# Performance work log

Measured on AMD Instinct MI355X. Metric: run time of the kernel, lower is better.

The kernel has to match this reference:

```python
import jax, jax.numpy as jnp
import numpy as np


def setup_inputs() -> dict:
    key = jax.random.key(0)
    k1, k2, k3, k4, k5 = jax.random.split(key, 5)
    b, n, L, D, m = 8, 8192, 512, 128, 16
    x = jax.random.normal(k1, (b, n, L), dtype=jnp.float32)
    # attention MLP: Linear(L->D, no bias), Tanh, Linear(D->1, no bias)
    W1 = jax.random.normal(k2, (L, D), dtype=jnp.float32) / np.sqrt(L).astype(np.float32)
    W2 = jax.random.normal(k3, (D, 1), dtype=jnp.float32) / np.sqrt(D).astype(np.float32)
    batched_image_ids = jax.random.randint(k4, (b, n), 0, m)  # which image each packed token belongs to
    key_pad_mask = jax.random.bernoulli(k5, 0.1, (b, n))      # True = padding token
    return {"x": x, "W1": W1, "W2": W2,
            "batched_image_ids": batched_image_ids,
            "key_pad_mask": key_pad_mask,
            "max_queries": 16}


def reference(x, W1, W2, batched_image_ids, key_pad_mask, max_queries):
    # Attention scores per token: tanh(x W1) W2 -> [b, n, 1]
    A = jnp.tanh(x @ W1) @ W2
    A = jnp.swapaxes(A, -1, -2)  # [b, 1, n]
    b, n, d = x.shape
    # Per-image pooling mask: token j contributes to query i iff its image id == i and not padded
    image_id_arange = jnp.arange(max_queries)                                    # [m]
    attn_pool_mask = (image_id_arange[None, :, None] == batched_image_ids[:, None, :])
    attn_pool_mask = attn_pool_mask & (~key_pad_mask)[:, None, :]                # [b, m, n]
    neg = -jnp.finfo(A.dtype).max
    A = jnp.where(attn_pool_mask, jnp.broadcast_to(A, (b, max_queries, n)), neg)
    A = jax.nn.softmax(A, axis=-1)                                               # [b, m, n]
    out = jnp.einsum('bmn,bnd->bmd', A, x)                                       # pooled per image
    # num_images == max_queries for every bag -> is_images selects everything
    out = out.reshape(b * max_queries, d)
    return out
```

## Files before the change

kernel.cpp:

```cpp
#include <hip/hip_runtime.h>
#include <hip/hip_bf16.h>
#include <cstdint>
#include <cstddef>

typedef __attribute__((ext_vector_type(8))) short bf16x8;
typedef __attribute__((ext_vector_type(4))) float f32x4;

#define BATCH 8
#define NTOK 8192
#define LDIM 512
#define DDIM 128
#define NQ 16
#define NSEG 8
#define SEGLEN (NTOK / NSEG)

static __device__ __forceinline__ short f2bf(float f) {
  uint32_t u = __float_as_uint(f);
  uint32_t r = u + 0x7fffu + ((u >> 16) & 1u);
  return (short)(r >> 16);
}

static __device__ __forceinline__ bf16x8 cvt8(float4 a, float4 b) {
  bf16x8 o;
  o[0] = f2bf(a.x); o[1] = f2bf(a.y); o[2] = f2bf(a.z); o[3] = f2bf(a.w);
  o[4] = f2bf(b.x); o[5] = f2bf(b.y); o[6] = f2bf(b.z); o[7] = f2bf(b.w);
  return o;
}

static __device__ __forceinline__ unsigned int flipf(float v) {
  unsigned int u = __float_as_uint(v);
  return (u & 0x80000000u) ? ~u : (u | 0x80000000u);
}
static __device__ __forceinline__ float unflipf(unsigned int u) {
  return __uint_as_float((u & 0x80000000u) ? (u & 0x7fffffffu) : ~u);
}

static __device__ __forceinline__ bool is_pad(const void* pad, int byteFlag, int j) {
  return byteFlag ? (((const unsigned char*)pad)[j] != 0)
                  : (((const int*)pad)[j] != 0);
}

__global__ __launch_bounds__(256) void k_detect(const unsigned int* __restrict__ pad_raw,
                                                int* __restrict__ flag,
                                                unsigned int* __restrict__ gmax) {
  if (threadIdx.x < 128) gmax[threadIdx.x] = 0u;
  int any_gt1 = 0;
  for (int i = threadIdx.x; i < 16384; i += 256)
    if (pad_raw[i] > 1u) any_gt1 = 1;
  unsigned long long m = __ballot(any_gt1);
  __shared__ int s[4];
  if ((threadIdx.x & 63) == 0) s[threadIdx.x >> 6] = (m != 0ull) ? 1 : 0;
  __syncthreads();
  if (threadIdx.x == 0) flag[0] = (s[0] | s[1] | s[2] | s[3]);
}

__global__ void k0_wfrag(const float* __restrict__ W1, short* __restrict__ wfrag) {
  int tid = blockIdx.x * blockDim.x + threadIdx.x;
  if (tid >= 16 * 8 * 64) return;
  int l = tid & 63;
  int t = (tid >> 6) & 7;
  int c = tid >> 9;
  int kbase = c * 32 + (l >> 4) * 8;
  int col = t * 16 + (l & 15);
  bf16x8 frag;
#pragma unroll
  for (int i = 0; i < 8; ++i) frag[i] = f2bf(W1[(size_t)(kbase + i) * DDIM + col]);
  ((bf16x8*)wfrag)[tid] = frag;
}

__global__ __launch_bounds__(512, 4) void k1_scores(const float* __restrict__ x,
                                                    const short* __restrict__ wfrag,
                                                    const float* __restrict__ W2,
                                                    const int* __restrict__ ids,
                                                    const void* __restrict__ pad,
                                                    const int* __restrict__ flag,
                                                    float* __restrict__ A,
                                                    unsigned int* __restrict__ gmax) {
  __shared__ short ldsw[32768];
  __shared__ unsigned int qmax[16];
  const int tid = threadIdx.x, wave = tid >> 6, lane = tid & 63;
  const int rowBase = blockIdx.x * 128 + wave * 16;
  const int b = rowBase >> 13;
  const float* xp = x + (size_t)(rowBase + (lane & 15)) * LDIM + ((lane >> 4) * 8);
  if (tid < 16) qmax[tid] = 0u;

#define STAGE(h)                                                                              \
  {                                                                                           \
    const unsigned int* src_ = (const unsigned int*)wfrag + (h) * 16384;                      \
    _Pragma("unroll")                                                                         \
    for (int i = 0; i < 8; ++i) {                                                             \
      __builtin_amdgcn_global_load_lds(                                                       \
          (const __attribute__((address_space(1))) unsigned int*)(src_ + (i * 512 + tid) * 4),\
          (__attribute__((address_space(3))) unsigned int*)&ldsw[(i * 512 + wave * 64) * 8],  \
          16, 0, 0);                                                                          \
    }                                                                                         \
  }

#define ALOAD(dst, c)                                  \
  {                                                    \
    dst[0] = *(const float4*)(xp + (c) * 32);          \
    dst[1] = *(const float4*)(xp + (c) * 32 + 4);      \
  }

  f32x4 acc[8];
#pragma unroll
  for (int t = 0; t < 8; ++t) acc[t] = (f32x4){0.f, 0.f, 0.f, 0.f};
  float4 avbuf[2][2];

  STAGE(0);
  ALOAD(avbuf[0], 0);
  ALOAD(avbuf[1], 1);
  __syncthreads();

#pragma unroll
  for (int cc = 0; cc < 8; ++cc) {
    bf16x8 af = cvt8(avbuf[cc & 1][0], avbuf[cc & 1][1]);
    if (cc < 6) ALOAD(avbuf[cc & 1], cc + 2);
#pragma unroll
    for (int t = 0; t < 8; ++t) {
      bf16x8 bfr = *(const bf16x8*)&ldsw[((cc * 8 + t) * 64 + lane) * 8];
      acc[t] = __builtin_amdgcn_mfma_f32_16x16x32_bf16(af, bfr, acc[t], 0, 0, 0);
    }
  }
  ALOAD(avbuf[0], 8);
  ALOAD(avbuf[1], 9);
  __syncthreads();
  STAGE(1);
  __syncthreads();

#pragma unroll
  for (int cc = 0; cc < 8; ++cc) {
    bf16x8 af = cvt8(avbuf[cc & 1][0], avbuf[cc & 1][1]);
    if (cc < 6) ALOAD(avbuf[cc & 1], 10 + cc);
#pragma unroll
    for (int t = 0; t < 8; ++t) {
      bf16x8 bfr = *(const bf16x8*)&ldsw[((cc * 8 + t) * 64 + lane) * 8];
      acc[t] = __builtin_amdgcn_mfma_f32_16x16x32_bf16(af, bfr, acc[t], 0, 0, 0);
    }
  }
#undef STAGE
#undef ALOAD

  float w2v[8];
#pragma unroll
  for (int t = 0; t < 8; ++t) w2v[t] = W2[t * 16 + (lane & 15)];
  const int bfl = flag[0];
  float asum[4] = {0.f, 0.f, 0.f, 0.f};
#pragma unroll
  for (int t = 0; t < 8; ++t) {
#pragma unroll
    for (int r = 0; r < 4; ++r) {
      float h = 1.f - 2.f / (__expf(2.f * acc[t][r]) + 1.f);
      asum[r] += h * w2v[t];
    }
  }
#pragma unroll
  for (int m = 1; m < 16; m <<= 1) {
#pragma unroll
    for (int r = 0; r < 4; ++r) asum[r] += __shfl_xor(asum[r], m, 64);
  }
  if ((lane & 15) == 0) {
    int rb = rowBase + (lane >> 4) * 4;
#pragma unroll
    for (int r = 0; r < 4; ++r) {
      int row = rb + r;
      float v = asum[r];
      A[row] = v;
      if (!is_pad(pad, bfl, row)) atomicMax(&qmax[ids[row]], flipf(v));
    }
  }
  __syncthreads();
  if (tid < 16 && qmax[tid] != 0u) atomicMax(&gmax[(b << 4) + tid], qmax[tid]);
}

__global__ __launch_bounds__(256) void k3_pool(const float* __restrict__ x,
                                               const float* __restrict__ A,
                                               const int* __restrict__ ids,
                                               const void* __restrict__ pad,
                                               const int* __restrict__ flag,
                                               const unsigned int* __restrict__ gmax,
                                               float* __restrict__ partial,
                                               float* __restrict__ wsum) {
  int blk = blockIdx.x;
  int s = blk & 7, q = (blk >> 3) & 15, b = blk >> 7;
  int wave = threadIdx.x >> 6, lane = threadIdx.x & 63;
  int bfl = flag[0];
  __shared__ float w_lds[1024];
  __shared__ unsigned short j_lds[1024];
  __shared__ int cnt[4];
  __shared__ float wred[4];

  unsigned int mraw = gmax[(b << 4) + q];
  float mx = (mraw == 0u) ? 0.f : unflipf(mraw);
  const int base = b * NTOK;

  int wbase = wave * 256;
  int wpos = wbase;
  float wacc = 0.f;
#pragma unroll
  for (int g = 0; g < 4; ++g) {
    int j = s * SEGLEN + wave * 256 + g * 64 + lane;
    bool mem = (ids[base + j] == q) && !is_pad(pad, bfl, base + j);
    float wt = mem ? __expf(A[base + j] - mx) : 0.f;
    wacc += wt;
    unsigned long long mask = __ballot(mem);
    if (mem) {
      int pos = wpos + __popcll(mask & ((1ull << lane) - 1ull));
      w_lds[pos] = wt;
      j_lds[pos] = (unsigned short)j;
    }
    wpos += __popcll(mask);
  }
#pragma unroll
  for (int m = 1; m < 64; m <<= 1) wacc += __shfl_xor(wacc, m, 64);
  if (lane == 0) { cnt[wave] = wpos - wbase; wred[wave] = wacc; }
  __syncthreads();

  int c0 = threadIdx.x * 2;
  float ax = 0.f, ay = 0.f;
  for (int w = 0; w < 4; ++w) {
    int nw = cnt[w];
#pragma unroll 2
    for (int e = 0; e < nw; ++e) {
      float wt = w_lds[w * 256 + e];
      int j = j_lds[w * 256 + e];
      const float* xr = x + (size_t)(base + j) * LDIM + c0;
      ax += wt * xr[0];
      ay += wt * xr[1];
    }
  }
  size_t po = (size_t)blk * LDIM + c0;
  partial[po] = ax;
  partial[po + 1] = ay;
  if (threadIdx.x == 0) wsum[blk] = wred[0] + wred[1] + wred[2] + wred[3];
}

__global__ void k4_reduce(const float* __restrict__ partial, const float* __restrict__ wsum,
                          float* __restrict__ out) {
  int e = blockIdx.x * blockDim.x + threadIdx.x;
  if (e >= BATCH * NQ * LDIM) return;
  int bi = e >> 9, c = e & 511;
  float ps = 0.f, ws = 0.f;
#pragma unroll
  for (int t = 0; t < 8; ++t) {
    ps += partial[(size_t)(bi * 8 + t) * LDIM + c];
    ws += wsum[bi * 8 + t];
  }
  out[e] = (ws > 0.f) ? (ps / ws) : 0.f;
}

extern "C" void kernel_launch(void* const* d_in, const int* in_sizes, int n_in,
                              void* d_out, int out_size, void* d_ws, size_t ws_size,
                              hipStream_t stream) {
  const float* x = (const float*)d_in[0];
  const float* W1 = (const float*)d_in[1];
  const float* W2 = (const float*)d_in[2];
  const int* ids = (const int*)d_in[3];
  const void* pad = d_in[4];
  float* out = (float*)d_out;

  char* ws = (char*)d_ws;
  short* wfrag = (short*)ws;
  float* A = (float*)(ws + 131072);
  unsigned int* gmax = (unsigned int*)(ws + 393216);
  float* wsum = (float*)(ws + 393728);
  int* flag = (int*)(ws + 397824);
  float* partial = (float*)(ws + 397952);

  hipLaunchKernelGGL(k_detect, dim3(1), dim3(256), 0, stream, (const unsigned int*)pad, flag, gmax);
  hipLaunchKernelGGL(k0_wfrag, dim3(32), dim3(256), 0, stream, W1, wfrag);
  hipLaunchKernelGGL(k1_scores, dim3((BATCH * NTOK) / 128), dim3(512), 0, stream,
                     x, wfrag, W2, ids, pad, flag, A, gmax);
  hipLaunchKernelGGL(k3_pool, dim3(BATCH * NQ * NSEG), dim3(256), 0, stream,
                     x, A, ids, pad, flag, gmax, partial, wsum);
  hipLaunchKernelGGL(k4_reduce, dim3((BATCH * NQ * LDIM) / 256), dim3(256), 0, stream,
                     partial, wsum, out);
}
```

Before: 71.63 us.

## Merge setup kernels, quarter W1 staging for occupancy, vectorize pooling gather

Merges the pad-detect kernel into the W1 fragment kernel, removing one launch. The scores kernel now stages W1 in four 32KB quarters instead of two 64KB halves, halving its LDS footprint and raising launch bounds to 6 blocks/CU, at the cost of extra barriers. The pooling kernel compacts member tokens into one contiguous list and splits it across two thread groups that load x with float4 instead of two scalar loads. The reduce kernel then sums twice as many partial rows.

After: 70.67 us. Within noise of the previous version (-1.3%).

```diff
diff --git a/kernel.cpp b/kernel.cpp
--- a/kernel.cpp
+++ b/kernel.cpp
@@ -40,35 +40,37 @@
                   : (((const int*)pad)[j] != 0);
 }
 
-__global__ __launch_bounds__(256) void k_detect(const unsigned int* __restrict__ pad_raw,
+__global__ __launch_bounds__(256) void k0_wfrag(const float* __restrict__ W1,
+                                                short* __restrict__ wfrag,
+                                                const unsigned int* __restrict__ pad_raw,
                                                 int* __restrict__ flag,
                                                 unsigned int* __restrict__ gmax) {
-  if (threadIdx.x < 128) gmax[threadIdx.x] = 0u;
-  int any_gt1 = 0;
-  for (int i = threadIdx.x; i < 16384; i += 256)
-    if (pad_raw[i] > 1u) any_gt1 = 1;
-  unsigned long long m = __ballot(any_gt1);
-  __shared__ int s[4];
-  if ((threadIdx.x & 63) == 0) s[threadIdx.x >> 6] = (m != 0ull) ? 1 : 0;
-  __syncthreads();
-  if (threadIdx.x == 0) flag[0] = (s[0] | s[1] | s[2] | s[3]);
-}
-
-__global__ void k0_wfrag(const float* __restrict__ W1, short* __restrict__ wfrag) {
   int tid = blockIdx.x * blockDim.x + threadIdx.x;
-  if (tid >= 16 * 8 * 64) return;
-  int l = tid & 63;
-  int t = (tid >> 6) & 7;
-  int c = tid >> 9;
-  int kbase = c * 32 + (l >> 4) * 8;
-  int col = t * 16 + (l & 15);
-  bf16x8 frag;
-#pragma unroll
-  for (int i = 0; i < 8; ++i) frag[i] = f2bf(W1[(size_t)(kbase + i) * DDIM + col]);
-  ((bf16x8*)wfrag)[tid] = frag;
-}
-
-__global__ __launch_bounds__(512, 4) void k1_scores(const float* __restrict__ x,
+  if (tid < 16 * 8 * 64) {
+    int l = tid & 63;
+    int t = (tid >> 6) & 7;
+    int c = tid >> 9;
+    int kbase = c * 32 + (l >> 4) * 8;
+    int col = t * 16 + (l & 15);
+    bf16x8 frag;
+#pragma unroll
+    for (int i = 0; i < 8; ++i) frag[i] = f2bf(W1[(size_t)(kbase + i) * DDIM + col]);
+    ((bf16x8*)wfrag)[tid] = frag;
+  }
+  if (blockIdx.x == 0) {
+    if (threadIdx.x < 128) gmax[threadIdx.x] = 0u;
+    int any_gt1 = 0;
+    for (int i = threadIdx.x; i < 16384; i += 256)
+      if (pad_raw[i] > 1u) any_gt1 = 1;
+    unsigned long long m = __ballot(any_gt1);
+    __shared__ int s[4];
+    if ((threadIdx.x & 63) == 0) s[threadIdx.x >> 6] = (m != 0ull) ? 1 : 0;
+    __syncthreads();
+    if (threadIdx.x == 0) flag[0] = (s[0] | s[1] | s[2] | s[3]);
+  }
+}
+
+__global__ __launch_bounds__(512, 6) void k1_scores(const float* __restrict__ x,
                                                     const short* __restrict__ wfrag,
                                                     const float* __restrict__ W2,
                                                     const int* __restrict__ ids,
@@ -76,7 +78,7 @@
                                                     const int* __restrict__ flag,
                                                     float* __restrict__ A,
                                                     unsigned int* __restrict__ gmax) {
-  __shared__ short ldsw[32768];
+  __shared__ short ldsw[16384];
   __shared__ unsigned int qmax[16];
   const int tid = threadIdx.x, wave = tid >> 6, lane = tid & 63;
   const int rowBase = blockIdx.x * 128 + wave * 16;
@@ -84,11 +86,11 @@
   const float* xp = x + (size_t)(rowBase + (lane & 15)) * LDIM + ((lane >> 4) * 8);
   if (tid < 16) qmax[tid] = 0u;
 
-#define STAGE(h)                                                                              \
+#define STAGE(qd)                                                                             \
   {                                                                                           \
-    const unsigned int* src_ = (const unsigned int*)wfrag + (h) * 16384;                      \
+    const unsigned int* src_ = (const unsigned int*)wfrag + (qd) * 8192;                      \
     _Pragma("unroll")                                                                         \
-    for (int i = 0; i < 8; ++i) {                                                             \
+    for (int i = 0; i < 4; ++i) {                                                             \
       __builtin_amdgcn_global_load_lds(                                                       \
           (const __attribute__((address_space(1))) unsigned int*)(src_ + (i * 512 + tid) * 4),\
           (__attribute__((address_space(3))) unsigned int*)&ldsw[(i * 512 + wave * 64) * 8],  \
@@ -113,29 +115,22 @@
   __syncthreads();
 
 #pragma unroll
-  for (int cc = 0; cc < 8; ++cc) {
-    bf16x8 af = cvt8(avbuf[cc & 1][0], avbuf[cc & 1][1]);
-    if (cc < 6) ALOAD(avbuf[cc & 1], cc + 2);
-#pragma unroll
-    for (int t = 0; t < 8; ++t) {
-      bf16x8 bfr = *(const bf16x8*)&ldsw[((cc * 8 + t) * 64 + lane) * 8];
-      acc[t] = __builtin_amdgcn_mfma_f32_16x16x32_bf16(af, bfr, acc[t], 0, 0, 0);
-    }
-  }
-  ALOAD(avbuf[0], 8);
-  ALOAD(avbuf[1], 9);
-  __syncthreads();
-  STAGE(1);
-  __syncthreads();
-
-#pragma unroll
-  for (int cc = 0; cc < 8; ++cc) {
-    bf16x8 af = cvt8(avbuf[cc & 1][0], avbuf[cc & 1][1]);
-    if (cc < 6) ALOAD(avbuf[cc & 1], 10 + cc);
-#pragma unroll
-    for (int t = 0; t < 8; ++t) {
-      bf16x8 bfr = *(const bf16x8*)&ldsw[((cc * 8 + t) * 64 + lane) * 8];
-      acc[t] = __builtin_amdgcn_mfma_f32_16x16x32_bf16(af, bfr, acc[t], 0, 0, 0);
+  for (int qd = 0; qd < 4; ++qd) {
+#pragma unroll
+    for (int cc = 0; cc < 4; ++cc) {
+      const int c = qd * 4 + cc;
+      bf16x8 af = cvt8(avbuf[c & 1][0], avbuf[c & 1][1]);
+      if (c < 14) ALOAD(avbuf[c & 1], c + 2);
+#pragma unroll
+      for (int t = 0; t < 8; ++t) {
+        bf16x8 bfr = *(const bf16x8*)&ldsw[((cc * 8 + t) * 64 + lane) * 8];
+        acc[t] = __builtin_amdgcn_mfma_f32_16x16x32_bf16(af, bfr, acc[t], 0, 0, 0);
+      }
+    }
+    if (qd < 3) {
+      __syncthreads();
+      STAGE(qd + 1);
+      __syncthreads();
     }
   }
 #undef STAGE
@@ -185,53 +180,64 @@
   int s = blk & 7, q = (blk >> 3) & 15, b = blk >> 7;
   int wave = threadIdx.x >> 6, lane = threadIdx.x & 63;
   int bfl = flag[0];
-  __shared__ float w_lds[1024];
-  __shared__ unsigned short j_lds[1024];
+  __shared__ float w_u[1024];
+  __shared__ unsigned short j_u[1024];
   __shared__ int cnt[4];
   __shared__ float wred[4];
 
   unsigned int mraw = gmax[(b << 4) + q];
   float mx = (mraw == 0u) ? 0.f : unflipf(mraw);
   const int base = b * NTOK;
-
-  int wbase = wave * 256;
-  int wpos = wbase;
+  const int tokBase = s * SEGLEN + wave * 256;
+
+  int myCnt = 0;
+#pragma unroll
+  for (int g = 0; g < 4; ++g) {
+    int j = tokBase + g * 64 + lane;
+    bool mem = (ids[base + j] == q) && !is_pad(pad, bfl, base + j);
+    myCnt += __popcll(__ballot(mem));
+  }
+  if (lane == 0) cnt[wave] = myCnt;
+  __syncthreads();
+
+  int wpos = 0;
+#pragma unroll
+  for (int w = 0; w < 4; ++w) if (w < wave) wpos += cnt[w];
+  const int total = cnt[0] + cnt[1] + cnt[2] + cnt[3];
+
   float wacc = 0.f;
 #pragma unroll
   for (int g = 0; g < 4; ++g) {
-    int j = s * SEGLEN + wave * 256 + g * 64 + lane;
+    int j = tokBase + g * 64 + lane;
     bool mem = (ids[base + j] == q) && !is_pad(pad, bfl, base + j);
     float wt = mem ? __expf(A[base + j] - mx) : 0.f;
     wacc += wt;
     unsigned long long mask = __ballot(mem);
     if (mem) {
       int pos = wpos + __popcll(mask & ((1ull << lane) - 1ull));
-      w_lds[pos] = wt;
-      j_lds[pos] = (unsigned short)j;
+      w_u[pos] = wt;
+      j_u[pos] = (unsigned short)j;
     }
     wpos += __popcll(mask);
   }
 #pragma unroll
   for (int m = 1; m < 64; m <<= 1) wacc += __shfl_xor(wacc, m, 64);
-  if (lane == 0) { cnt[wave] = wpos - wbase; wred[wave] = wacc; }
-  __syncthreads();
-
-  int c0 = threadIdx.x * 2;
-  float ax = 0.f, ay = 0.f;
-  for (int w = 0; w < 4; ++w) {
-    int nw = cnt[w];
-#pragma unroll 2
-    for (int e = 0; e < nw; ++e) {
-      float wt = w_lds[w * 256 + e];
-      int j = j_lds[w * 256 + e];
-      const float* xr = x + (size_t)(base + j) * LDIM + c0;
-      ax += wt * xr[0];
-      ay += wt * xr[1];
-    }
-  }
-  size_t po = (size_t)blk * LDIM + c0;
-  partial[po] = ax;
-  partial[po + 1] = ay;
+  if (lane == 0) wred[wave] = wacc;
+  __syncthreads();
+
+  int grp = threadIdx.x >> 7, ct = threadIdx.x & 127;
+  int c0 = ct * 4;
+  int half = (total + 1) >> 1;
+  int e0 = grp ? half : 0;
+  int e1 = grp ? total : half;
+  float4 av = {0.f, 0.f, 0.f, 0.f};
+  for (int e = e0; e < e1; ++e) {
+    float wt = w_u[e];
+    int j = j_u[e];
+    float4 xr = *(const float4*)(x + (size_t)(base + j) * LDIM + c0);
+    av.x += wt * xr.x; av.y += wt * xr.y; av.z += wt * xr.z; av.w += wt * xr.w;
+  }
+  *(float4*)(partial + ((size_t)(blk * 2 + grp)) * LDIM + c0) = av;
   if (threadIdx.x == 0) wsum[blk] = wred[0] + wred[1] + wred[2] + wred[3];
 }
 
@@ -242,10 +248,9 @@
   int bi = e >> 9, c = e & 511;
   float ps = 0.f, ws = 0.f;
 #pragma unroll
-  for (int t = 0; t < 8; ++t) {
-    ps += partial[(size_t)(bi * 8 + t) * LDIM + c];
-    ws += wsum[bi * 8 + t];
-  }
+  for (int t = 0; t < 16; ++t) ps += partial[(size_t)(bi * 16 + t) * LDIM + c];
+#pragma unroll
+  for (int t = 0; t < 8; ++t) ws += wsum[bi * 8 + t];
   out[e] = (ws > 0.f) ? (ps / ws) : 0.f;
 }
 
@@ -267,8 +272,8 @@
   int* flag = (int*)(ws + 397824);
   float* partial = (float*)(ws + 397952);
 
-  hipLaunchKernelGGL(k_detect, dim3(1), dim3(256), 0, stream, (const unsigned int*)pad, flag, gmax);
-  hipLaunchKernelGGL(k0_wfrag, dim3(32), dim3(256), 0, stream, W1, wfrag);
+  hipLaunchKernelGGL(k0_wfrag, dim3(32), dim3(256), 0, stream,
+                     W1, wfrag, (const unsigned int*)pad, flag, gmax);
   hipLaunchKernelGGL(k1_scores, dim3((BATCH * NTOK) / 128), dim3(512), 0, stream,
                      x, wfrag, W2, ids, pad, flag, A, gmax);
   hipLaunchKernelGGL(k3_pool, dim3(BATCH * NQ * NSEG), dim3(256), 0, stream,
```
